# Performance work log

Measured on AMD Instinct MI355X. Metric: run time of the kernel, lower is better.

## Reference

```python
import jax, jax.numpy as jnp
import numpy as np

N_NODES = 100000
N_EDGES = 1600000
HIDDEN = 128
EPS = 0.0


def setup_inputs() -> dict:
    key = jax.random.key(0)
    ks = jax.random.split(key, 9)
    scale = 0.02
    x = jax.random.normal(ks[0], (N_NODES, HIDDEN), dtype=jnp.float32)
    edge_index = jax.random.randint(ks[1], (2, N_EDGES), 0, N_NODES, dtype=jnp.int64)
    edge_weight = jax.random.uniform(ks[2], (N_EDGES,), dtype=jnp.float32)
    # edge_encoder: nn.Linear(1, HIDDEN) -> weight [HIDDEN,1] stored as vector [HIDDEN]
    w_edge = jax.random.normal(ks[3], (HIDDEN,), dtype=jnp.float32) * scale
    b_edge = jnp.zeros((HIDDEN,), dtype=jnp.float32)
    # update_mlp: Linear(H,H) -> ReLU -> Linear(H,H); torch Linear weight is [out,in]
    w1 = jax.random.normal(ks[4], (HIDDEN, HIDDEN), dtype=jnp.float32) * scale
    b1 = jnp.zeros((HIDDEN,), dtype=jnp.float32)
    w2 = jax.random.normal(ks[5], (HIDDEN, HIDDEN), dtype=jnp.float32) * scale
    b2 = jnp.zeros((HIDDEN,), dtype=jnp.float32)
    return {"x": x, "edge_index": edge_index, "edge_weight": edge_weight,
            "w_edge": w_edge, "b_edge": b_edge,
            "w1": w1, "b1": b1, "w2": w2, "b2": b2}


def reference(x, edge_index, edge_weight, w_edge, b_edge, w1, b1, w2, b2):
    src_idx = edge_index[0]
    dst_idx = edge_index[1]
    # edge_encoder(edge_weight[:, None]): [E, H]
    edge_attr = edge_weight[:, None] * w_edge[None, :] + b_edge[None, :]
    # gather src node features + edge bias: [E, H]
    src_features = x[src_idx] + edge_attr
    # scatter-add into per-node buffer: [N, H]
    out = jax.ops.segment_sum(src_features, dst_idx, num_segments=x.shape[0])
    out = out + (1.0 + EPS) * x
    # update_mlp
    out = jax.nn.relu(out @ w1.T + b1) @ w2.T + b2
    return out
```

## Files before the change

kernel.cpp:

```cpp
#include <hip/hip_runtime.h>

#define HID    128
#define LDSW   136
#define NMAX   100000
#define BSH    8
#define BNODES 256
#define NBMAX  ((NMAX + BNODES - 1) / BNODES)
#define CAP    8192
#define EPB    2048
#define BCS    16
#define QCAP   2048
#define SRCPAD 3072
#define S8     (5.5f / 127.0f)

typedef __attribute__((ext_vector_type(8))) short bf16x8;
typedef __attribute__((ext_vector_type(4))) short s16x4;
typedef __attribute__((ext_vector_type(4))) float f32x4;

__device__ int           g_bcur[NBMAX * BCS];
__device__ int           g_erec[(size_t)NBMAX * CAP];
__device__ short         g_A[(size_t)NMAX * HID];
__device__ unsigned char g_x8[(size_t)(NMAX + 1) * HID];
__device__ short         g_w1p[HID * HID];
__device__ short         g_w2p[HID * HID];

__device__ __forceinline__ short f2bf(float f) {
    unsigned u = __builtin_bit_cast(unsigned, f);
    unsigned r = (u + 0x7fffu + ((u >> 16) & 1u)) >> 16;
    return (short)r;
}
__device__ __forceinline__ unsigned q8(float f) {
    int t = (int)rintf(f * (127.0f / 5.5f)) + 128;
    t = t < 0 ? 0 : (t > 255 ? 255 : t);
    return (unsigned)t;
}

__global__ __launch_bounds__(256) void xcast_kernel(const float* __restrict__ x,
                                                    int n16r, int n16z) {
    int i = blockIdx.x * 256 + threadIdx.x;
    if (i >= n16z) return;
    int4 pk = { 0, 0, 0, 0 };
    if (i < n16r) {
        const float4* p = (const float4*)(x + (size_t)i * 16);
        float4 v0 = p[0], v1 = p[1], v2 = p[2], v3 = p[3];
        pk.x = (int)(q8(v0.x) | (q8(v0.y) << 8) | (q8(v0.z) << 16) | (q8(v0.w) << 24));
        pk.y = (int)(q8(v1.x) | (q8(v1.y) << 8) | (q8(v1.z) << 16) | (q8(v1.w) << 24));
        pk.z = (int)(q8(v2.x) | (q8(v2.y) << 8) | (q8(v2.z) << 16) | (q8(v2.w) << 24));
        pk.w = (int)(q8(v3.x) | (q8(v3.y) << 8) | (q8(v3.z) << 16) | (q8(v3.w) << 24));
    }
    ((int4*)g_x8)[i] = pk;
}

__global__ __launch_bounds__(256) void wpack_kernel(const float* __restrict__ w1,
                                                    const float* __restrict__ w2) {
    int id = blockIdx.x * 256 + threadIdx.x;
    const float* w = (id & 2048) ? w2 : w1;
    short* dst = (id & 2048) ? g_w2p : g_w1p;
    int e = id & 2047;
    int lane = e & 63, kk = (e >> 6) & 3, nt = e >> 8;
    int row = nt * 16 + (lane & 15);
    int col = kk * 32 + (lane >> 4) * 8;
    float4 a = *(const float4*)(w + row * HID + col);
    float4 b = *(const float4*)(w + row * HID + col + 4);
    bf16x8 pk = { f2bf(a.x), f2bf(a.y), f2bf(a.z), f2bf(a.w),
                  f2bf(b.x), f2bf(b.y), f2bf(b.z), f2bf(b.w) };
    *(bf16x8*)(dst + e * 8) = pk;
}

__global__ __launch_bounds__(256) void init_bcur(int nb) {
    int i = blockIdx.x * 256 + threadIdx.x;
    if (i < nb) g_bcur[i * BCS] = i * CAP;
}

__global__ __launch_bounds__(256) void bucket_scatter(
    const int* __restrict__ ei, const float* __restrict__ ew, int nEdges, int nb)
{
    __shared__ int   hist[NBMAX];
    __shared__ int   s_rec[EPB];
    __shared__ short s_b[EPB];
    const int tid = threadIdx.x;
    const int e0 = blockIdx.x * EPB;
    const int cnt = min(EPB, nEdges - e0);

    for (int b = tid; b < nb; b += 256) hist[b] = 0;
    __syncthreads();

    for (int k = tid; k < cnt; k += 256) {
        int e = e0 + k;
        int s = ei[e];
        int d = ei[nEdges + e];
        int bb = d >> BSH;
        int q7 = (int)(ew[e] * 127.0f + 0.5f);
        s_rec[k] = s | ((d & (BNODES - 1)) << 17) | (q7 << 25);
        s_b[k] = (short)bb;
        atomicAdd(&hist[bb], 1);
    }
    __syncthreads();

    for (int b = tid; b < nb; b += 256) {
        int c = hist[b];
        hist[b] = (c > 0) ? atomicAdd(&g_bcur[b * BCS], c) : 0;
    }
    __syncthreads();

    for (int k = tid; k < cnt; k += 256) {
        int rec = s_rec[k];
        int b = s_b[k];
        int slot = atomicAdd(&hist[b], 1);
        slot = min(slot, (b + 1) * CAP - 1);
        g_erec[slot] = rec;
    }
}

__global__ __launch_bounds__(256) void aggregate_kernel(
    const float* __restrict__ w_edge, const float* __restrict__ b_edge, int nNodes)
{
    __shared__ int s_q[QCAP];
    __shared__ int s_src[SRCPAD];
    __shared__ int s_poff[64 + 1];
    __shared__ int s_hist[64];
    __shared__ int s_rank[64];
    __shared__ int s_sumq[64];
    __shared__ int s_qn;

    const int tid = threadIdx.x;
    const int lane = tid & 63;
    const int wave = tid >> 6;
    const int blk = blockIdx.x;
    const int bb = blk >> 2;
    const int qq = blk & 3;
    const int node0 = (bb << BSH) + (qq << 6);
    const int base = bb * CAP;
    const int cnt = min(g_bcur[bb * BCS] - base, CAP);

    if (tid < 64) { s_hist[tid] = 0; s_rank[tid] = 0; s_sumq[tid] = 0; }
    if (tid == 0) s_qn = 0;
    __syncthreads();

    const int g = lane >> 3;
    const int l16 = (lane & 7) * 16;
    const int fidx = ((lane & 7) * 8 + g) * 2;
    const float2 we2 = *(const float2*)(w_edge + fidx);
    const float2 be2 = *(const float2*)(b_edge + fidx);
    const int b1 = (lane >> 4) & 1;
    const int b2 = (lane >> 5) & 1;
    const int hsh = (g & 1) * 16;

    for (int e = tid; e < cnt; e += 256) {
        int rec = g_erec[base + e];
        bool mine = (((rec >> 23) & 3) == qq);
        unsigned long long m = __ballot(mine);
        int tot = __popcll(m);
        int wb = 0;
        if (lane == 0 && tot) wb = atomicAdd(&s_qn, tot);
        wb = __shfl(wb, 0, 64);
        if (mine) {
            int rank = __builtin_amdgcn_mbcnt_hi((unsigned)(m >> 32),
                        __builtin_amdgcn_mbcnt_lo((unsigned)m, 0));
            int qi = wb + rank;
            if (qi < QCAP) {
                s_q[qi] = rec;
                int lg = (rec >> 17) & 63;
                atomicAdd(&s_hist[lg], 1);
                atomicAdd(&s_sumq[lg], (int)((unsigned)rec >> 25));
            }
        }
    }
    __syncthreads();
    const int qn = min(s_qn, QCAP);

    if (tid < 64) {
        int v = s_hist[tid];
        int p = (v + 16) & ~15;
        int pincl = p;
        #pragma unroll
        for (int d = 1; d < 64; d <<= 1) {
            int t = __shfl_up(pincl, d, 64);
            if (tid >= d) pincl += t;
        }
        s_poff[tid] = pincl - p;
        if (tid == 63) s_poff[64] = pincl;
    }
    for (int k = tid; k < SRCPAD; k += 256) s_src[k] = nNodes;
    __syncthreads();

    if (tid < 64) s_src[s_poff[tid] + s_hist[tid]] = min(node0 + tid, nNodes);
    for (int k = tid; k < qn; k += 256) {
        int rec = s_q[k];
        int loc = (rec >> 17) & 63;
        int r = atomicAdd(&s_rank[loc], 1);
        int idx = min(s_poff[loc] + r, SRCPAD - 1);
        s_src[idx] = rec & 0x1FFFF;
    }
    __syncthreads();

    const unsigned M = 0x00FF00FFu;
    for (int i = 0; i < 16; ++i) {
        int nl = wave * 16 + i;
        int node = node0 + nl;
        int p0 = s_poff[nl], p1 = s_poff[nl + 1];
        unsigned A[8] = { 0, 0, 0, 0, 0, 0, 0, 0 };
        for (int j = p0; j < p1; j += 16) {
            int s0 = s_src[j + g];
            int s1 = s_src[j + 8 + g];
            int4 d0 = *(const int4*)(g_x8 + (s0 << 7) + l16);
            int4 d1 = *(const int4*)(g_x8 + (s1 << 7) + l16);
            unsigned u;
            u = (unsigned)d0.x; A[0] += u & M; A[1] += (u >> 8) & M;
            u = (unsigned)d0.y; A[2] += u & M; A[3] += (u >> 8) & M;
            u = (unsigned)d0.z; A[4] += u & M; A[5] += (u >> 8) & M;
            u = (unsigned)d0.w; A[6] += u & M; A[7] += (u >> 8) & M;
            u = (unsigned)d1.x; A[0] += u & M; A[1] += (u >> 8) & M;
            u = (unsigned)d1.y; A[2] += u & M; A[3] += (u >> 8) & M;
            u = (unsigned)d1.z; A[4] += u & M; A[5] += (u >> 8) & M;
            u = (unsigned)d1.w; A[6] += u & M; A[7] += (u >> 8) & M;
        }

        unsigned k0 = b1 ? A[2] : A[0];
        unsigned k1 = b1 ? A[3] : A[1];
        unsigned k2 = b1 ? A[6] : A[4];
        unsigned k3 = b1 ? A[7] : A[5];
        unsigned t0 = b1 ? A[0] : A[2];
        unsigned t1 = b1 ? A[1] : A[3];
        unsigned t2 = b1 ? A[4] : A[6];
        unsigned t3 = b1 ? A[5] : A[7];
        k0 += __shfl_xor(t0, 16, 64);
        k1 += __shfl_xor(t1, 16, 64);
        k2 += __shfl_xor(t2, 16, 64);
        k3 += __shfl_xor(t3, 16, 64);
        unsigned m0 = b2 ? k2 : k0;
        unsigned m1 = b2 ? k3 : k1;
        unsigned u0 = b2 ? k0 : k2;
        unsigned u1 = b2 ? k1 : k3;
        m0 += __shfl_xor(u0, 32, 64);
        m1 += __shfl_xor(u1, 32, 64);
        m0 += __shfl_xor(m0, 8, 64);
        m1 += __shfl_xor(m1, 8, 64);

        float f0 = (float)((m0 >> hsh) & 0xFFFFu);
        float f1 = (float)((m1 >> hsh) & 0xFFFFu);
        float dg = (float)s_hist[nl];
        float sw_ = (float)s_sumq[nl] * (1.0f / 127.0f);
        float cc = -128.0f * S8 * (dg + 1.0f);
        float o0 = S8 * f0 + cc + sw_ * we2.x + dg * be2.x;
        float o1 = S8 * f1 + cc + sw_ * we2.y + dg * be2.y;
        unsigned pk = ((unsigned)(unsigned short)f2bf(o0)) |
                      ((unsigned)(unsigned short)f2bf(o1) << 16);
        if (node < nNodes)
            *(unsigned*)(g_A + (node << 7) + fidx) = pk;
    }
}

__global__ __launch_bounds__(256) void mlp_kernel(
    const float* __restrict__ b1, const float* __restrict__ b2,
    float* __restrict__ out, int nNodes, int nTiles)
{
    __shared__ __align__(16) short W1s[HID * HID];
    __shared__ __align__(16) short W2s[HID * HID];
    __shared__ __align__(16) short As[32 * LDSW];

    const int tid = threadIdx.x;
    const int lane = tid & 63;
    const int wave = tid >> 6;
    const int l15 = lane & 15;
    const int quad = lane >> 4;
    const int mrow = (wave & 1) * 16;
    const int ntg0 = (wave >> 1) * 4;

    for (int it = 0; it < 8; ++it) {
        int idx = it * 256 + tid;
        ((int4*)W1s)[idx] = ((const int4*)g_w1p)[idx];
        ((int4*)W2s)[idx] = ((const int4*)g_w2p)[idx];
    }

    float bias1[4], bias2[4];
    #pragma unroll
    for (int nt = 0; nt < 4; ++nt) {
        bias1[nt] = b1[(ntg0 + nt) * 16 + l15];
        bias2[nt] = b2[(ntg0 + nt) * 16 + l15];
    }
    __syncthreads();

    for (int t = blockIdx.x; t < nTiles; t += gridDim.x) {
        int node0 = t * 32;
        for (int it = 0; it < 2; ++it) {
            int idx = it * 256 + tid;
            int r = idx >> 4, c = idx & 15;
            int node = node0 + r;
            int4 v = { 0, 0, 0, 0 };
            if (node < nNodes) v = ((const int4*)(g_A + (size_t)node * HID))[c];
            *(int4*)(As + r * LDSW + c * 8) = v;
        }
        __syncthreads();

        bf16x8 af[4];
        #pragma unroll
        for (int k = 0; k < 4; ++k)
            af[k] = *(const bf16x8*)(As + (mrow + l15) * LDSW + k * 32 + quad * 8);
        f32x4 acc[4];
        #pragma unroll
        for (int nt = 0; nt < 4; ++nt) acc[nt] = (f32x4){0.f, 0.f, 0.f, 0.f};
        #pragma unroll
        for (int nt = 0; nt < 4; ++nt)
            #pragma unroll
            for (int k = 0; k < 4; ++k) {
                bf16x8 bf = *(const bf16x8*)(W1s + (((ntg0 + nt) * 4 + k) * 64 + lane) * 8);
                acc[nt] = __builtin_amdgcn_mfma_f32_16x16x32_bf16(af[k], bf, acc[nt], 0, 0, 0);
            }
        __syncthreads();

        #pragma unroll
        for (int nt = 0; nt < 4; ++nt) {
            int col = (ntg0 + nt) * 16 + l15;
            #pragma unroll
            for (int r = 0; r < 4; ++r) {
                float h = acc[nt][r] + bias1[nt];
                h = h > 0.f ? h : 0.f;
                As[(mrow + quad * 4 + r) * LDSW + col] = f2bf(h);
            }
        }
        __syncthreads();

        #pragma unroll
        for (int k = 0; k < 4; ++k)
            af[k] = *(const bf16x8*)(As + (mrow + l15) * LDSW + k * 32 + quad * 8);
        f32x4 acc2[4];
        #pragma unroll
        for (int nt = 0; nt < 4; ++nt) acc2[nt] = (f32x4){0.f, 0.f, 0.f, 0.f};
        #pragma unroll
        for (int nt = 0; nt < 4; ++nt)
            #pragma unroll
            for (int k = 0; k < 4; ++k) {
                bf16x8 bf = *(const bf16x8*)(W2s + (((ntg0 + nt) * 4 + k) * 64 + lane) * 8);
                acc2[nt] = __builtin_amdgcn_mfma_f32_16x16x32_bf16(af[k], bf, acc2[nt], 0, 0, 0);
            }

        #pragma unroll
        for (int nt = 0; nt < 4; ++nt) {
            int col = (ntg0 + nt) * 16 + l15;
            #pragma unroll
            for (int r = 0; r < 4; ++r) {
                int node = node0 + mrow + quad * 4 + r;
                if (node < nNodes)
                    out[(size_t)node * HID + col] = acc2[nt][r] + bias2[nt];
            }
        }
        __syncthreads();
    }
}

extern "C" void kernel_launch(void* const* d_in, const int* in_sizes, int n_in,
                              void* d_out, int out_size, void* d_ws, size_t ws_size,
                              hipStream_t stream) {
    const float* x      = (const float*)d_in[0];
    const int*   ei     = (const int*)d_in[1];
    const float* ew     = (const float*)d_in[2];
    const float* w_edge = (const float*)d_in[3];
    const float* b_edge = (const float*)d_in[4];
    const float* w1     = (const float*)d_in[5];
    const float* b1     = (const float*)d_in[6];
    const float* w2     = (const float*)d_in[7];
    const float* b2     = (const float*)d_in[8];
    float* out = (float*)d_out;

    int nNodes = in_sizes[0] / HID;
    int nEdges = in_sizes[2];
    int nb = (nNodes + BNODES - 1) >> BSH;
    int nTiles = (nNodes + 31) / 32;

    int n16r = nNodes * (HID / 16);
    int n16z = (nNodes + 1) * (HID / 16);
    xcast_kernel<<<(n16z + 255) / 256, 256, 0, stream>>>(x, n16r, n16z);
    wpack_kernel<<<16, 256, 0, stream>>>(w1, w2);
    init_bcur<<<(nb + 255) / 256, 256, 0, stream>>>(nb);
    bucket_scatter<<<(nEdges + EPB - 1) / EPB, 256, 0, stream>>>(ei, ew, nEdges, nb);
    aggregate_kernel<<<nb * 4, 256, 0, stream>>>(w_edge, b_edge, nNodes);
    mlp_kernel<<<512, 256, 0, stream>>>(b1, b2, out, nNodes, nTiles);
}
```

Measured before the change: 244.6 us.

## Prefetch next node's first gather chunk and drop LDS edge queue

Removes the shared-memory edge queue: the bucket's edge records are read from global memory twice, once to build histograms and once to scatter source indices, instead of being staged in LDS. The gather loop now handles 32 neighbours per step, padding each node's list to a multiple of 32, and loads the first chunk of the next node before reducing the current one, so memory latency overlaps with the shuffle reduction. SRCPAD grows to hold the larger padding. The cost is more padded dummy loads (for ~16-degree nodes, often 32 slots where 16 would do) and a second pass over the edge records in global memory.

Measured after the change: 249.6 us. 1.02x slower.

```diff
diff --git a/kernel.cpp b/kernel.cpp
--- a/kernel.cpp
+++ b/kernel.cpp
@@ -9,8 +9,7 @@
 #define CAP    8192
 #define EPB    2048
 #define BCS    16
-#define QCAP   2048
-#define SRCPAD 3072
+#define SRCPAD 4096
 #define S8     (5.5f / 127.0f)
 
 typedef __attribute__((ext_vector_type(8))) short bf16x8;
@@ -115,13 +114,11 @@
 __global__ __launch_bounds__(256) void aggregate_kernel(
     const float* __restrict__ w_edge, const float* __restrict__ b_edge, int nNodes)
 {
-    __shared__ int s_q[QCAP];
     __shared__ int s_src[SRCPAD];
     __shared__ int s_poff[64 + 1];
     __shared__ int s_hist[64];
     __shared__ int s_rank[64];
     __shared__ int s_sumq[64];
-    __shared__ int s_qn;
 
     const int tid = threadIdx.x;
     const int lane = tid & 63;
@@ -134,7 +131,6 @@
     const int cnt = min(g_bcur[bb * BCS] - base, CAP);
 
     if (tid < 64) { s_hist[tid] = 0; s_rank[tid] = 0; s_sumq[tid] = 0; }
-    if (tid == 0) s_qn = 0;
     __syncthreads();
 
     const int g = lane >> 3;
@@ -148,30 +144,17 @@
 
     for (int e = tid; e < cnt; e += 256) {
         int rec = g_erec[base + e];
-        bool mine = (((rec >> 23) & 3) == qq);
-        unsigned long long m = __ballot(mine);
-        int tot = __popcll(m);
-        int wb = 0;
-        if (lane == 0 && tot) wb = atomicAdd(&s_qn, tot);
-        wb = __shfl(wb, 0, 64);
-        if (mine) {
-            int rank = __builtin_amdgcn_mbcnt_hi((unsigned)(m >> 32),
-                        __builtin_amdgcn_mbcnt_lo((unsigned)m, 0));
-            int qi = wb + rank;
-            if (qi < QCAP) {
-                s_q[qi] = rec;
-                int lg = (rec >> 17) & 63;
-                atomicAdd(&s_hist[lg], 1);
-                atomicAdd(&s_sumq[lg], (int)((unsigned)rec >> 25));
-            }
-        }
-    }
-    __syncthreads();
-    const int qn = min(s_qn, QCAP);
+        if (((rec >> 23) & 3) == qq) {
+            int lg = (rec >> 17) & 63;
+            atomicAdd(&s_hist[lg], 1);
+            atomicAdd(&s_sumq[lg], (int)((unsigned)rec >> 25));
+        }
+    }
+    __syncthreads();
 
     if (tid < 64) {
         int v = s_hist[tid];
-        int p = (v + 16) & ~15;
+        int p = (v + 32) & ~31;
         int pincl = p;
         #pragma unroll
         for (int d = 1; d < 64; d <<= 1) {
@@ -184,46 +167,63 @@
     for (int k = tid; k < SRCPAD; k += 256) s_src[k] = nNodes;
     __syncthreads();
 
-    if (tid < 64) s_src[s_poff[tid] + s_hist[tid]] = min(node0 + tid, nNodes);
-    for (int k = tid; k < qn; k += 256) {
-        int rec = s_q[k];
-        int loc = (rec >> 17) & 63;
-        int r = atomicAdd(&s_rank[loc], 1);
-        int idx = min(s_poff[loc] + r, SRCPAD - 1);
-        s_src[idx] = rec & 0x1FFFF;
+    if (tid < 64)
+        s_src[min(s_poff[tid] + s_hist[tid], SRCPAD - 1)] = min(node0 + tid, nNodes);
+    for (int e = tid; e < cnt; e += 256) {
+        int rec = g_erec[base + e];
+        if (((rec >> 23) & 3) == qq) {
+            int loc = (rec >> 17) & 63;
+            int r = atomicAdd(&s_rank[loc], 1);
+            int idx = min(s_poff[loc] + r, SRCPAD - 1);
+            s_src[idx] = rec & 0x1FFFF;
+        }
     }
     __syncthreads();
 
     const unsigned M = 0x00FF00FFu;
+#define ACC(dd) { unsigned u;                                      \
+        u = (unsigned)(dd).x; A0 += u & M; A1 += (u >> 8) & M;     \
+        u = (unsigned)(dd).y; A2 += u & M; A3 += (u >> 8) & M;     \
+        u = (unsigned)(dd).z; A4 += u & M; A5 += (u >> 8) & M;     \
+        u = (unsigned)(dd).w; A6 += u & M; A7 += (u >> 8) & M; }
+
+    const int nlw = wave * 16;
+    int p0 = min(s_poff[nlw], SRCPAD - 32);
+    int p1 = min(s_poff[nlw + 1], SRCPAD - 32);
+    int4 d0 = *(const int4*)(g_x8 + (s_src[p0 + g] << 7) + l16);
+    int4 d1 = *(const int4*)(g_x8 + (s_src[p0 + 8 + g] << 7) + l16);
+    int4 d2 = *(const int4*)(g_x8 + (s_src[p0 + 16 + g] << 7) + l16);
+    int4 d3 = *(const int4*)(g_x8 + (s_src[p0 + 24 + g] << 7) + l16);
+
     for (int i = 0; i < 16; ++i) {
-        int nl = wave * 16 + i;
+        int nl = nlw + i;
         int node = node0 + nl;
-        int p0 = s_poff[nl], p1 = s_poff[nl + 1];
-        unsigned A[8] = { 0, 0, 0, 0, 0, 0, 0, 0 };
-        for (int j = p0; j < p1; j += 16) {
-            int s0 = s_src[j + g];
-            int s1 = s_src[j + 8 + g];
-            int4 d0 = *(const int4*)(g_x8 + (s0 << 7) + l16);
-            int4 d1 = *(const int4*)(g_x8 + (s1 << 7) + l16);
-            unsigned u;
-            u = (unsigned)d0.x; A[0] += u & M; A[1] += (u >> 8) & M;
-            u = (unsigned)d0.y; A[2] += u & M; A[3] += (u >> 8) & M;
-            u = (unsigned)d0.z; A[4] += u & M; A[5] += (u >> 8) & M;
-            u = (unsigned)d0.w; A[6] += u & M; A[7] += (u >> 8) & M;
-            u = (unsigned)d1.x; A[0] += u & M; A[1] += (u >> 8) & M;
-            u = (unsigned)d1.y; A[2] += u & M; A[3] += (u >> 8) & M;
-            u = (unsigned)d1.z; A[4] += u & M; A[5] += (u >> 8) & M;
-            u = (unsigned)d1.w; A[6] += u & M; A[7] += (u >> 8) & M;
-        }
-
-        unsigned k0 = b1 ? A[2] : A[0];
-        unsigned k1 = b1 ? A[3] : A[1];
-        unsigned k2 = b1 ? A[6] : A[4];
-        unsigned k3 = b1 ? A[7] : A[5];
-        unsigned t0 = b1 ? A[0] : A[2];
-        unsigned t1 = b1 ? A[1] : A[3];
-        unsigned t2 = b1 ? A[4] : A[6];
-        unsigned t3 = b1 ? A[5] : A[7];
+        unsigned A0 = 0, A1 = 0, A2 = 0, A3 = 0, A4 = 0, A5 = 0, A6 = 0, A7 = 0;
+        ACC(d0); ACC(d1); ACC(d2); ACC(d3);
+        for (int j = p0 + 32; j < p1; j += 32) {
+            int4 e0 = *(const int4*)(g_x8 + (s_src[j + g] << 7) + l16);
+            int4 e1 = *(const int4*)(g_x8 + (s_src[j + 8 + g] << 7) + l16);
+            int4 e2 = *(const int4*)(g_x8 + (s_src[j + 16 + g] << 7) + l16);
+            int4 e3 = *(const int4*)(g_x8 + (s_src[j + 24 + g] << 7) + l16);
+            ACC(e0); ACC(e1); ACC(e2); ACC(e3);
+        }
+        int np1 = p1;
+        if (i < 15) {
+            np1 = min(s_poff[nl + 2], SRCPAD - 32);
+            d0 = *(const int4*)(g_x8 + (s_src[p1 + g] << 7) + l16);
+            d1 = *(const int4*)(g_x8 + (s_src[p1 + 8 + g] << 7) + l16);
+            d2 = *(const int4*)(g_x8 + (s_src[p1 + 16 + g] << 7) + l16);
+            d3 = *(const int4*)(g_x8 + (s_src[p1 + 24 + g] << 7) + l16);
+        }
+
+        unsigned k0 = b1 ? A2 : A0;
+        unsigned k1 = b1 ? A3 : A1;
+        unsigned k2 = b1 ? A6 : A4;
+        unsigned k3 = b1 ? A7 : A5;
+        unsigned t0 = b1 ? A0 : A2;
+        unsigned t1 = b1 ? A1 : A3;
+        unsigned t2 = b1 ? A4 : A6;
+        unsigned t3 = b1 ? A5 : A7;
         k0 += __shfl_xor(t0, 16, 64);
         k1 += __shfl_xor(t1, 16, 64);
         k2 += __shfl_xor(t2, 16, 64);
@@ -248,7 +248,10 @@
                       ((unsigned)(unsigned short)f2bf(o1) << 16);
         if (node < nNodes)
             *(unsigned*)(g_A + (node << 7) + fidx) = pk;
-    }
+
+        p0 = p1; p1 = np1;
+    }
+#undef ACC
 }
 
 __global__ __launch_bounds__(256) void mlp_kernel(
```
